# Optimization experiments

Measured on AMD Instinct MI355X. Metric: run time of the kernel, lower is better.

The kernel has to match this reference:

```python
import jax, jax.numpy as jnp
import numpy as np
import math

# dims (scaled-down DeepSeek-MLA-style config)
DIM = 2048
NH = 16
QLR = 768       # dla_q_lora_rank
KVLR = 512      # dla_kv_lora_rank
DN = 128        # qk_nope_head_dim
DR = 64         # qk_rope_head_dim
DV = 128        # v_head_dim
QKH = DN + DR   # 192
BSZ = 1
SEQ = 2048
LAYER_IDX = 3
LAMBDA_INIT = 0.8 - 0.6 * math.exp(-0.3 * LAYER_IDX)
SCALE = QKH ** -0.5  # max_seq_len == original_seq_len -> no mscale correction
MAX_SCORE = 100.0


def apply_rope(x, cos, sin):
    # x: [b, s, h, d]; consecutive pairs (x[2i], x[2i+1]) form complex numbers
    xr, xi = x[..., 0::2], x[..., 1::2]
    c = cos[None, :, None, :]
    sn = sin[None, :, None, :]
    yr = xr * c - xi * sn
    yi = xr * sn + xi * c
    return jnp.stack([yr, yi], axis=-1).reshape(x.shape)


def setup_inputs() -> dict:
    key = jax.random.key(0)
    ks = jax.random.split(key, 12)
    x = jax.random.normal(ks[0], (BSZ, SEQ, DIM), dtype=jnp.float32)
    s = 0.02
    wq_a = jax.random.normal(ks[1], (QLR, DIM), dtype=jnp.float32) * s
    wq_b = jax.random.normal(ks[2], (NH * QKH, QLR), dtype=jnp.float32) * s
    wkv_a = jax.random.normal(ks[3], (KVLR + DR, DIM), dtype=jnp.float32) * s
    wkv_b = jax.random.normal(ks[4], (NH * (DN + DV), KVLR), dtype=jnp.float32) * s
    wo = jax.random.normal(ks[5], (DIM, NH * DV), dtype=jnp.float32) * s
    lambda_q_nope = jax.random.normal(ks[6], (DN,), dtype=jnp.float32) * 0.1
    lambda_q_rope = jax.random.normal(ks[7], (DR,), dtype=jnp.float32) * 0.1
    lambda_k_nope = jax.random.normal(ks[8], (DN,), dtype=jnp.float32) * 0.1
    lambda_k_rope = jax.random.normal(ks[9], (DR,), dtype=jnp.float32) * 0.1
    # rope frequencies
    inv_freq = 1.0 / (10000.0 ** (np.arange(0, DR, 2, dtype=np.float32) / DR))
    angles = np.arange(SEQ, dtype=np.float32)[:, None] * inv_freq[None, :]
    freqs_cos = jnp.asarray(np.cos(angles))
    freqs_sin = jnp.asarray(np.sin(angles))
    # causal mask (prefill, start_pos = 0)
    mask = jnp.where(jnp.tril(jnp.ones((SEQ, SEQ), dtype=bool)), 0.0, -1e9).astype(jnp.float32)
    return {
        'x': x, 'wq_a': wq_a, 'wq_b': wq_b, 'wkv_a': wkv_a, 'wkv_b': wkv_b, 'wo': wo,
        'lambda_q_nope': lambda_q_nope, 'lambda_q_rope': lambda_q_rope,
        'lambda_k_nope': lambda_k_nope, 'lambda_k_rope': lambda_k_rope,
        'freqs_cos': freqs_cos, 'freqs_sin': freqs_sin, 'mask': mask, 'start_pos': 0,
    }


def reference(x, wq_a, wq_b, wkv_a, wkv_b, wo,
              lambda_q_nope, lambda_q_rope, lambda_k_nope, lambda_k_rope,
              freqs_cos, freqs_sin, mask, start_pos):
    b, s, _ = x.shape
    # differential-attention lambda scalar
    lam = (jnp.exp(jnp.dot(lambda_q_nope, lambda_k_nope))
           - jnp.exp(jnp.dot(lambda_q_rope, lambda_k_rope)) + LAMBDA_INIT)
    # low-rank q projection
    q = (x @ wq_a.T) @ wq_b.T                    # [b, s, NH*QKH]
    q = q.reshape(b, s, NH, QKH)
    q_nope, q_pe = q[..., :DN], q[..., DN:]
    q_pe = apply_rope(q_pe, freqs_cos, freqs_sin)
    # compressed kv + shared rope key
    kv_full = x @ wkv_a.T                        # [b, s, KVLR + DR]
    kv, k_pe = kv_full[..., :KVLR], kv_full[..., KVLR:]
    k_pe = apply_rope(k_pe[:, :, None, :], freqs_cos, freqs_sin)  # [b, s, 1, DR]
    kvb = (kv @ wkv_b.T).reshape(b, s, NH, DN + DV)
    k_nope, v = kvb[..., :DN], kvb[..., DN:]
    q_full = jnp.concatenate([q_nope, q_pe], axis=-1)             # [b, s, NH, 192]
    k_full = jnp.concatenate([k_nope, jnp.broadcast_to(k_pe, (b, s, NH, DR))], axis=-1)
    # differential split into two halves of qk_head_dim//2 = 96
    H = QKH // 2
    q1, q2 = q_full[..., :H], q_full[..., H:]
    k1, k2 = k_full[..., :H], k_full[..., H:]
    s1 = jnp.einsum('bshd,bthd->bhst', q1, k1) * SCALE
    s2 = jnp.einsum('bshd,bthd->bhst', q2, k2) * SCALE
    s1 = jnp.clip(s1, -MAX_SCORE, MAX_SCORE) + mask[None, None]
    s2 = jnp.clip(s2, -MAX_SCORE, MAX_SCORE) + mask[None, None]
    attn = jax.nn.softmax(s1, axis=-1) - lam * jax.nn.softmax(s2, axis=-1)
    out = jnp.einsum('bhst,bthd->bshd', attn, v)  # [b, s, NH, DV]
    out = out * (1.0 - LAMBDA_INIT)
    return out.reshape(b, s, NH * DV) @ wo.T
```

## Files before the change

### kernel.cpp

```cpp
#include <hip/hip_runtime.h>
#include <stdint.h>

#define SEQ   2048
#define NH    16
#define DIMM  2048
#define QLR   768
#define KVLR  512
#define DN    128
#define DR    64
#define DV    128
#define QKH   192
#define KVPAD 640
#define SCALE_F 0.07216878364870323f
#define LAM_INIT 0.5560582f
#define C1F      0.4439418f
#define PSTR  36

typedef __attribute__((ext_vector_type(8))) uint16_t u16x8;
typedef __attribute__((ext_vector_type(8))) __bf16   bf16x8;
typedef __attribute__((ext_vector_type(4))) float    f32x4;

#define MFMA16(a,b,c) __builtin_amdgcn_mfma_f32_16x16x32_bf16((a),(b),(c),0,0,0)

__device__ __forceinline__ uint16_t f2bf(float f){ uint32_t x; __builtin_memcpy(&x,&f,4); return (uint16_t)((x + 0x7FFFu + ((x>>16)&1u))>>16); }
__device__ __forceinline__ bf16x8 ldfrag(const uint16_t* p){ return __builtin_bit_cast(bf16x8, *(const u16x8*)p); }
__device__ __forceinline__ void gload_lds16(const uint16_t* g, uint16_t* l){
  __builtin_amdgcn_global_load_lds((const __attribute__((address_space(1))) void*)g,
                                   (__attribute__((address_space(3))) void*)l, 16, 0, 0);
}
__device__ __forceinline__ void stor(uint16_t* p, float v){ *p = f2bf(v); }
__device__ __forceinline__ void stor(float* p, float v){ *p = v; }

__global__ void cvt(const float* __restrict__ in, uint16_t* __restrict__ outp){
  int i = (blockIdx.x*256 + threadIdx.x)*8;
  float4 a = *(const float4*)(in + i);
  float4 b = *(const float4*)(in + i + 4);
  u16x8 r;
  r[0]=f2bf(a.x); r[1]=f2bf(a.y); r[2]=f2bf(a.z); r[3]=f2bf(a.w);
  r[4]=f2bf(b.x); r[5]=f2bf(b.y); r[6]=f2bf(b.z); r[7]=f2bf(b.w);
  *(u16x8*)(outp + i) = r;
}

__global__ void pad_wkva(const float* __restrict__ in, uint16_t* __restrict__ outp){
  int idx = blockIdx.x*256 + threadIdx.x;
  int n = idx >> 11;
  outp[idx] = (n < 576) ? f2bf(in[idx]) : (uint16_t)0;
}

template <typename OT>
__global__ __launch_bounds__(256) void gemm_bt(const uint16_t* __restrict__ A, int lda,
                                               const uint16_t* __restrict__ B,
                                               OT* __restrict__ C, int ldc, int K)
{
  __shared__ __align__(16) uint16_t As[128*32];
  __shared__ __align__(16) uint16_t Bs[128*32];
  const int tid  = threadIdx.x;
  const int wid  = tid >> 6;
  const int lane = tid & 63;
  const int wr   = (wid >> 1) * 64;
  const int wc   = (wid & 1) * 64;
  const int srow = lane >> 2;
  const int scol = (lane & 3) * 8;
  const uint16_t* Abase = A + (size_t)(blockIdx.x * 128) * lda;
  const uint16_t* Bbase = B + (size_t)(blockIdx.y * 128) * K;
  f32x4 acc[4][4] = {};
  for (int k0 = 0; k0 < K; k0 += 32) {
    __syncthreads();
#pragma unroll
    for (int c = 0; c < 2; ++c) {
      int r = (wid*2 + c)*16 + srow;
      gload_lds16(Abase + (size_t)r*lda + k0 + scol, &As[(wid*2 + c)*512]);
      gload_lds16(Bbase + (size_t)r*K   + k0 + scol, &Bs[(wid*2 + c)*512]);
    }
    __syncthreads();
    bf16x8 af[4], bfr[4];
#pragma unroll
    for (int m = 0; m < 4; ++m)
      af[m] = ldfrag(&As[(wr + m*16 + (lane&15))*32 + ((lane>>4)*8)]);
#pragma unroll
    for (int n = 0; n < 4; ++n)
      bfr[n] = ldfrag(&Bs[(wc + n*16 + (lane&15))*32 + ((lane>>4)*8)]);
#pragma unroll
    for (int m = 0; m < 4; ++m)
#pragma unroll
      for (int n = 0; n < 4; ++n)
        acc[m][n] = MFMA16(af[m], bfr[n], acc[m][n]);
  }
  const int rbase = blockIdx.x*128 + wr + ((lane>>4)<<2);
  const int cbase = blockIdx.y*128 + wc + (lane&15);
#pragma unroll
  for (int m = 0; m < 4; ++m)
#pragma unroll
    for (int n = 0; n < 4; ++n)
#pragma unroll
      for (int r = 0; r < 4; ++r)
        stor(&C[(size_t)(rbase + m*16 + r)*ldc + cbase + n*16], acc[m][n][r]);
}

__global__ void lam_kernel(const float* lqn, const float* lqr,
                           const float* lkn, const float* lkr, float* outp){
  if (threadIdx.x == 0 && blockIdx.x == 0) {
    float d1 = 0.f, d2 = 0.f;
    for (int i = 0; i < DN; ++i) d1 += lqn[i] * lkn[i];
    for (int i = 0; i < DR; ++i) d2 += lqr[i] * lkr[i];
    outp[0] = __expf(d1) - __expf(d2) + LAM_INIT;
  }
}

__global__ void rope_q(uint16_t* __restrict__ q, const float* __restrict__ cs,
                       const float* __restrict__ sn){
  int idx = blockIdx.x*256 + threadIdx.x;
  int j = idx & 31, hh = (idx>>5) & 15, s = idx >> 9;
  uint16_t* p = q + (size_t)s*(NH*QKH) + hh*QKH + DN + 2*j;
  float xr = (float)__builtin_bit_cast(__bf16, p[0]);
  float xi = (float)__builtin_bit_cast(__bf16, p[1]);
  float c = cs[s*32+j], si = sn[s*32+j];
  p[0] = f2bf(xr*c - xi*si);
  p[1] = f2bf(xr*si + xi*c);
}

__global__ void mat_k(const uint16_t* __restrict__ kvb, const uint16_t* __restrict__ kvf,
                      const float* __restrict__ cs, const float* __restrict__ sn,
                      uint16_t* __restrict__ kfull){
  int idx = blockIdx.x*256 + threadIdx.x;
  int d = idx % QKH; int th = idx / QKH; int t = th & 2047; int hh = th >> 11;
  uint16_t val;
  if (d < DN) {
    val = kvb[(size_t)t*4096 + hh*256 + d];
  } else {
    int dd = d - DN, j = dd >> 1;
    float xr = (float)__builtin_bit_cast(__bf16, kvf[(size_t)t*KVPAD + KVLR + 2*j]);
    float xi = (float)__builtin_bit_cast(__bf16, kvf[(size_t)t*KVPAD + KVLR + 2*j + 1]);
    float c = cs[t*32+j], si = sn[t*32+j];
    val = f2bf((dd & 1) ? (xr*si + xi*c) : (xr*c - xi*si));
  }
  kfull[idx] = val;
}

__global__ void mat_v(const uint16_t* __restrict__ kvb, uint16_t* __restrict__ vtp){
  int idx = blockIdx.x*256 + threadIdx.x;
  int t = idx & 2047, d = (idx>>11) & 127, hh = idx >> 18;
  vtp[idx] = kvb[(size_t)t*4096 + hh*256 + DN + d];
}

__device__ __forceinline__ void proc_set(f32x4 s[2], float m[4], float l[4], f32x4 O[8],
                                         uint16_t* pl, int qrow0, int t0, int subrow, int l15)
{
#pragma unroll
  for (int half = 0; half < 2; ++half)
#pragma unroll
    for (int r = 0; r < 4; ++r) {
      float v = s[half][r] * SCALE_F;
      v = fminf(fmaxf(v, -100.f), 100.f);
      if (t0 + half*16 + l15 > qrow0 + subrow + r) v = -1e30f;
      s[half][r] = v;
    }
  float corr[4];
#pragma unroll
  for (int r = 0; r < 4; ++r) {
    float tm = fmaxf(s[0][r], s[1][r]);
#pragma unroll
    for (int off = 1; off < 16; off <<= 1) tm = fmaxf(tm, __shfl_xor(tm, off, 64));
    float mn = fmaxf(m[r], tm);
    corr[r] = __expf(m[r] - mn);
    m[r] = mn;
  }
#pragma unroll
  for (int r = 0; r < 4; ++r) {
    s[0][r] = __expf(s[0][r] - m[r]);
    s[1][r] = __expf(s[1][r] - m[r]);
    float rs = s[0][r] + s[1][r];
#pragma unroll
    for (int off = 1; off < 16; off <<= 1) rs += __shfl_xor(rs, off, 64);
    l[r] = l[r]*corr[r] + rs;
  }
#pragma unroll
  for (int n = 0; n < 8; ++n)
#pragma unroll
    for (int r = 0; r < 4; ++r) O[n][r] *= corr[r];
#pragma unroll
  for (int half = 0; half < 2; ++half)
#pragma unroll
    for (int r = 0; r < 4; ++r)
      pl[(subrow + r)*PSTR + half*16 + l15] = f2bf(s[half][r]);
}

__global__ __launch_bounds__(256, 2) void attn_kernel(
    const uint16_t* __restrict__ q,
    const uint16_t* __restrict__ kf,
    const uint16_t* __restrict__ vt,
    const float* __restrict__ lamp,
    uint16_t* __restrict__ o)
{
  __shared__ __align__(16) uint16_t P_lds[4][2][16*PSTR];
  const int b  = blockIdx.x;
  const int h  = b & 15;
  const int j  = (b >> 4) & 15;
  const int qb = (b < 256) ? j : (31 - j);
  const int wid  = threadIdx.x >> 6;
  const int lane = threadIdx.x & 63;
  const int l15 = lane & 15;
  const int lhi = lane >> 4;
  const int subrow = lhi * 4;
  const int qrow0 = qb*64 + wid*16;
  const float lam = lamp[0];

  bf16x8 qf[6];
  {
    const uint16_t* qbase = q + (size_t)(qrow0 + l15)*(NH*QKH) + h*QKH + lhi*8;
#pragma unroll
    for (int kb = 0; kb < 6; ++kb) qf[kb] = ldfrag(qbase + kb*32);
  }
  f32x4 O1[8] = {}, O2[8] = {};
  float m1[4], m2[4], l1[4], l2[4];
#pragma unroll
  for (int r = 0; r < 4; ++r) { m1[r] = m2[r] = -1e30f; l1[r] = l2[r] = 0.f; }

  const uint16_t* kbase = kf + (size_t)h*SEQ*QKH;
  const uint16_t* vbase = vt + (size_t)h*DV*SEQ;
  uint16_t* pl0 = &P_lds[wid][0][0];
  uint16_t* pl1 = &P_lds[wid][1][0];

  for (int t0 = 0; t0 < qrow0 + 16; t0 += 32) {
    bf16x8 kf0[6], kf1[6], vf[8];
    {
      const uint16_t* kp0 = kbase + (size_t)(t0 + l15)*QKH + lhi*8;
      const uint16_t* kp1 = kbase + (size_t)(t0 + 16 + l15)*QKH + lhi*8;
#pragma unroll
      for (int kb = 0; kb < 6; ++kb) { kf0[kb] = ldfrag(kp0 + kb*32); kf1[kb] = ldfrag(kp1 + kb*32); }
#pragma unroll
      for (int n = 0; n < 8; ++n) vf[n] = ldfrag(vbase + (size_t)(n*16 + l15)*SEQ + t0 + lhi*8);
    }
    f32x4 s1[2] = {}, s2[2] = {};
    __builtin_amdgcn_s_setprio(1);
#pragma unroll
    for (int kb = 0; kb < 3; ++kb) { s1[0] = MFMA16(qf[kb], kf0[kb], s1[0]); s1[1] = MFMA16(qf[kb], kf1[kb], s1[1]); }
#pragma unroll
    for (int kb = 3; kb < 6; ++kb) { s2[0] = MFMA16(qf[kb], kf0[kb], s2[0]); s2[1] = MFMA16(qf[kb], kf1[kb], s2[1]); }
    __builtin_amdgcn_s_setprio(0);

    proc_set(s1, m1, l1, O1, pl0, qrow0, t0, subrow, l15);
    proc_set(s2, m2, l2, O2, pl1, qrow0, t0, subrow, l15);

    asm volatile("s_waitcnt lgkmcnt(0)" ::: "memory");
    __builtin_amdgcn_sched_barrier(0);

    bf16x8 pf0 = ldfrag(&pl0[l15*PSTR + lhi*8]);
    bf16x8 pf1 = ldfrag(&pl1[l15*PSTR + lhi*8]);
    __builtin_amdgcn_s_setprio(1);
#pragma unroll
    for (int n = 0; n < 8; ++n) {
      O1[n] = MFMA16(pf0, vf[n], O1[n]);
      O2[n] = MFMA16(pf1, vf[n], O2[n]);
    }
    __builtin_amdgcn_s_setprio(0);
  }
#pragma unroll
  for (int r = 0; r < 4; ++r) {
    float inv1 = 1.f / l1[r], inv2 = lam / l2[r];
#pragma unroll
    for (int n = 0; n < 8; ++n) {
      float val = (O1[n][r]*inv1 - O2[n][r]*inv2) * C1F;
      o[(size_t)(qrow0 + subrow + r)*(NH*DV) + h*DV + n*16 + l15] = f2bf(val);
    }
  }
}

extern "C" void kernel_launch(void* const* d_in, const int* in_sizes, int n_in,
                              void* d_out, int out_size, void* d_ws, size_t ws_size,
                              hipStream_t stream)
{
  const float* x     = (const float*)d_in[0];
  const float* wq_a  = (const float*)d_in[1];
  const float* wq_b  = (const float*)d_in[2];
  const float* wkv_a = (const float*)d_in[3];
  const float* wkv_b = (const float*)d_in[4];
  const float* wo    = (const float*)d_in[5];
  const float* lqn   = (const float*)d_in[6];
  const float* lqr   = (const float*)d_in[7];
  const float* lkn   = (const float*)d_in[8];
  const float* lkr   = (const float*)d_in[9];
  const float* fcos  = (const float*)d_in[10];
  const float* fsin  = (const float*)d_in[11];

  char* ws = (char*)d_ws;
  size_t off = 0;
  float*    lam    = (float*)(ws + off);  off += 256;
  uint16_t* xb     = (uint16_t*)(ws + off); off += (size_t)DIMM*DIMM*2;
  uint16_t* wqab   = (uint16_t*)(ws + off); off += (size_t)QLR*DIMM*2;
  uint16_t* wqbb   = (uint16_t*)(ws + off); off += (size_t)NH*QKH*QLR*2;
  uint16_t* wkvap  = (uint16_t*)(ws + off); off += (size_t)KVPAD*DIMM*2;
  uint16_t* wkvbb  = (uint16_t*)(ws + off); off += (size_t)4096*KVLR*2;
  uint16_t* wob    = (uint16_t*)(ws + off); off += (size_t)DIMM*DIMM*2;
  uint16_t* qlat   = (uint16_t*)(ws + off); off += (size_t)SEQ*QLR*2;
  uint16_t* qbuf   = (uint16_t*)(ws + off); off += (size_t)SEQ*NH*QKH*2;
  uint16_t* kvfull = (uint16_t*)(ws + off); off += (size_t)SEQ*KVPAD*2;
  uint16_t* kvb    = (uint16_t*)(ws + off); off += (size_t)SEQ*4096*2;
  uint16_t* kfull  = (uint16_t*)(ws + off); off += (size_t)NH*SEQ*QKH*2;
  uint16_t* vtb    = (uint16_t*)(ws + off); off += (size_t)NH*DV*SEQ*2;
  uint16_t* attn   = (uint16_t*)(ws + off); off += (size_t)SEQ*NH*DV*2;

  lam_kernel<<<1, 64, 0, stream>>>(lqn, lqr, lkn, lkr, lam);
  cvt<<<2048, 256, 0, stream>>>(x, xb);
  cvt<<< 768, 256, 0, stream>>>(wq_a, wqab);
  cvt<<<1152, 256, 0, stream>>>(wq_b, wqbb);
  cvt<<<1024, 256, 0, stream>>>(wkv_b, wkvbb);
  cvt<<<2048, 256, 0, stream>>>(wo, wob);
  pad_wkva<<<5120, 256, 0, stream>>>(wkv_a, wkvap);

  gemm_bt<<<dim3(16, 6), 256, 0, stream>>>(xb, DIMM, wqab, qlat, QLR, DIMM);
  gemm_bt<<<dim3(16, 24), 256, 0, stream>>>(qlat, QLR, wqbb, qbuf, NH*QKH, QLR);
  rope_q<<<4096, 256, 0, stream>>>(qbuf, fcos, fsin);
  gemm_bt<<<dim3(16, 5), 256, 0, stream>>>(xb, DIMM, wkvap, kvfull, KVPAD, DIMM);
  gemm_bt<<<dim3(16, 32), 256, 0, stream>>>(kvfull, KVPAD, wkvbb, kvb, 4096, KVLR);
  mat_k<<<24576, 256, 0, stream>>>(kvb, kvfull, fcos, fsin, kfull);
  mat_v<<<16384, 256, 0, stream>>>(kvb, vtb);
  attn_kernel<<<512, 256, 0, stream>>>(qbuf, kfull, vtb, lam, attn);
  gemm_bt<<<dim3(16, 16), 256, 0, stream>>>(attn, NH*DV, wob, (float*)d_out, DIMM, DIMM);
}
```

Baseline: 385.6 us.

## Use single-wave attention blocks with double-buffered K register prefetch

```diff
diff --git a/kernel.cpp b/kernel.cpp
--- a/kernel.cpp
+++ b/kernel.cpp
@@ -185,24 +185,23 @@
       pl[(subrow + r)*PSTR + half*16 + l15] = f2bf(s[half][r]);
 }
 
-__global__ __launch_bounds__(256, 2) void attn_kernel(
+__global__ __launch_bounds__(64, 2) void attn_kernel(
     const uint16_t* __restrict__ q,
     const uint16_t* __restrict__ kf,
     const uint16_t* __restrict__ vt,
     const float* __restrict__ lamp,
     uint16_t* __restrict__ o)
 {
-  __shared__ __align__(16) uint16_t P_lds[4][2][16*PSTR];
+  __shared__ __align__(16) uint16_t P_lds[2][16*PSTR];
   const int b  = blockIdx.x;
   const int h  = b & 15;
-  const int j  = (b >> 4) & 15;
-  const int qb = (b < 256) ? j : (31 - j);
-  const int wid  = threadIdx.x >> 6;
+  const int c  = b >> 4;
   const int lane = threadIdx.x & 63;
   const int l15 = lane & 15;
   const int lhi = lane >> 4;
   const int subrow = lhi * 4;
-  const int qrow0 = qb*64 + wid*16;
+  const int qrow0 = c * 16;
+  const int kend  = qrow0 + 16;
   const float lam = lamp[0];
 
   bf16x8 qf[6];
@@ -218,25 +217,26 @@
 
   const uint16_t* kbase = kf + (size_t)h*SEQ*QKH;
   const uint16_t* vbase = vt + (size_t)h*DV*SEQ;
-  uint16_t* pl0 = &P_lds[wid][0][0];
-  uint16_t* pl1 = &P_lds[wid][1][0];
-
-  for (int t0 = 0; t0 < qrow0 + 16; t0 += 32) {
-    bf16x8 kf0[6], kf1[6], vf[8];
-    {
-      const uint16_t* kp0 = kbase + (size_t)(t0 + l15)*QKH + lhi*8;
-      const uint16_t* kp1 = kbase + (size_t)(t0 + 16 + l15)*QKH + lhi*8;
-#pragma unroll
-      for (int kb = 0; kb < 6; ++kb) { kf0[kb] = ldfrag(kp0 + kb*32); kf1[kb] = ldfrag(kp1 + kb*32); }
-#pragma unroll
-      for (int n = 0; n < 8; ++n) vf[n] = ldfrag(vbase + (size_t)(n*16 + l15)*SEQ + t0 + lhi*8);
-    }
+  uint16_t* pl0 = &P_lds[0][0];
+  uint16_t* pl1 = &P_lds[1][0];
+
+  auto loadK = [&](bf16x8 (&k0)[6], bf16x8 (&k1)[6], int t){
+    const uint16_t* kp0 = kbase + (size_t)(t + l15)*QKH + lhi*8;
+    const uint16_t* kp1 = kp0 + (size_t)16*QKH;
+#pragma unroll
+    for (int kb = 0; kb < 6; ++kb) { k0[kb] = ldfrag(kp0 + kb*32); k1[kb] = ldfrag(kp1 + kb*32); }
+  };
+
+  auto body = [&](bf16x8 (&k0)[6], bf16x8 (&k1)[6], int t0){
+    bf16x8 vf[8];
+#pragma unroll
+    for (int n = 0; n < 8; ++n) vf[n] = ldfrag(vbase + (size_t)(n*16 + l15)*SEQ + t0 + lhi*8);
     f32x4 s1[2] = {}, s2[2] = {};
     __builtin_amdgcn_s_setprio(1);
 #pragma unroll
-    for (int kb = 0; kb < 3; ++kb) { s1[0] = MFMA16(qf[kb], kf0[kb], s1[0]); s1[1] = MFMA16(qf[kb], kf1[kb], s1[1]); }
-#pragma unroll
-    for (int kb = 3; kb < 6; ++kb) { s2[0] = MFMA16(qf[kb], kf0[kb], s2[0]); s2[1] = MFMA16(qf[kb], kf1[kb], s2[1]); }
+    for (int kb = 0; kb < 3; ++kb) { s1[0] = MFMA16(qf[kb], k0[kb], s1[0]); s1[1] = MFMA16(qf[kb], k1[kb], s1[1]); }
+#pragma unroll
+    for (int kb = 3; kb < 6; ++kb) { s2[0] = MFMA16(qf[kb], k0[kb], s2[0]); s2[1] = MFMA16(qf[kb], k1[kb], s2[1]); }
     __builtin_amdgcn_s_setprio(0);
 
     proc_set(s1, m1, l1, O1, pl0, qrow0, t0, subrow, l15);
@@ -254,7 +254,20 @@
       O2[n] = MFMA16(pf1, vf[n], O2[n]);
     }
     __builtin_amdgcn_s_setprio(0);
-  }
+  };
+
+  bf16x8 ka0[6], ka1[6], kb0[6], kb1[6];
+  loadK(ka0, ka1, 0);
+  int t0 = 0;
+  while (true) {
+    loadK(kb0, kb1, t0 + 32);
+    body(ka0, ka1, t0);
+    t0 += 32; if (t0 >= kend) break;
+    loadK(ka0, ka1, t0 + 32);
+    body(kb0, kb1, t0);
+    t0 += 32; if (t0 >= kend) break;
+  }
+
 #pragma unroll
   for (int r = 0; r < 4; ++r) {
     float inv1 = 1.f / l1[r], inv2 = lam / l2[r];
@@ -315,6 +328,6 @@
   gemm_bt<<<dim3(16, 32), 256, 0, stream>>>(kvfull, KVPAD, wkvbb, kvb, 4096, KVLR);
   mat_k<<<24576, 256, 0, stream>>>(kvb, kvfull, fcos, fsin, kfull);
   mat_v<<<16384, 256, 0, stream>>>(kvb, vtb);
-  attn_kernel<<<512, 256, 0, stream>>>(qbuf, kfull, vtb, lam, attn);
+  attn_kernel<<<2048, 64, 0, stream>>>(qbuf, kfull, vtb, lam, attn);
   gemm_bt<<<dim3(16, 16), 256, 0, stream>>>(attn, NH*DV, wob, (float*)d_out, DIMM, DIMM);
 }
```

New measurement: 504.3 us. +30.8%, slower.
